# Kernel tuning notes

Measured on AMD Instinct MI355X. Metric: run time of the kernel, lower is better.

Reference implementation:

```python
import jax, jax.numpy as jnp
import numpy as np

EMBED_DIM = 1024
NUM_HEADS = 16
HEAD_DIM = EMBED_DIM // NUM_HEADS


def setup_inputs() -> dict:
    key = jax.random.key(0)
    ks = jax.random.split(key, 9)
    s = 1.0 / np.sqrt(EMBED_DIM)
    x = jax.random.normal(ks[0], (2, 2048, EMBED_DIM), dtype=jnp.float32)
    Wq = jax.random.uniform(ks[1], (EMBED_DIM, EMBED_DIM), jnp.float32, -s, s)
    bq = jax.random.uniform(ks[2], (EMBED_DIM,), jnp.float32, -s, s)
    Wk = jax.random.uniform(ks[3], (EMBED_DIM, EMBED_DIM), jnp.float32, -s, s)
    bk = jax.random.uniform(ks[4], (EMBED_DIM,), jnp.float32, -s, s)
    Wv = jax.random.uniform(ks[5], (EMBED_DIM, EMBED_DIM), jnp.float32, -s, s)
    bv = jax.random.uniform(ks[6], (EMBED_DIM,), jnp.float32, -s, s)
    Wo = jax.random.uniform(ks[7], (EMBED_DIM, EMBED_DIM), jnp.float32, -s, s)
    bo = jax.random.uniform(ks[8], (EMBED_DIM,), jnp.float32, -s, s)
    return {"x": x, "Wq": Wq, "bq": bq, "Wk": Wk, "bk": bk,
            "Wv": Wv, "bv": bv, "Wo": Wo, "bo": bo}


def reference(x, Wq, bq, Wk, bk, Wv, bv, Wo, bo):
    B, S, E = x.shape
    H, D = NUM_HEADS, HEAD_DIM
    # Linear projections (torch Linear: y = x @ W.T + b; here W stored as [in,out])
    Q = (x @ Wq + bq).reshape(B, S, H, D).transpose(0, 2, 1, 3)  # [B,H,S,D]
    K = (x @ Wk + bk).reshape(B, S, H, D).transpose(0, 2, 1, 3)
    V = (x @ Wv + bv).reshape(B, S, H, D).transpose(0, 2, 1, 3)
    scale = jnp.sqrt(jnp.asarray(D, dtype=jnp.float32))
    energy = jnp.einsum("bhqd,bhkd->bhqk", Q, K) / scale  # [B,H,S,S]
    attn = jax.nn.softmax(energy, axis=-1)
    out = jnp.einsum("bhqk,bhkd->bhqd", attn, V)  # [B,H,S,D]
    out = out.transpose(0, 2, 1, 3).reshape(B, S, E)
    return out @ Wo + bo
```

## Files before the change

kernel.cpp:

```cpp
#include <hip/hip_runtime.h>
#include <cstdint>
#include <cstddef>

#define S_LEN 2048
#define NHEAD 16
#define HDIM  64
#define EMB   1024
#define MROWS 4096
#define KDIM  1024

typedef __bf16 bf16;
typedef unsigned int u32;
typedef __attribute__((ext_vector_type(8)))  __bf16 bf16x8;
typedef __attribute__((ext_vector_type(4)))  __bf16 bf16x4;
typedef __attribute__((ext_vector_type(4)))  float  f32x4;
typedef __attribute__((ext_vector_type(16))) float  f32x16;
typedef __attribute__((ext_vector_type(4)))  u32    u32x4;

__device__ __forceinline__ f32x4 mfma_16x16x32(bf16x8 a, bf16x8 b, f32x4 c) {
  return __builtin_amdgcn_mfma_f32_16x16x32_bf16(a, b, c, 0, 0, 0);
}
__device__ __forceinline__ f32x16 mfma32(bf16x8 a, bf16x8 b, f32x16 c) {
  return __builtin_amdgcn_mfma_f32_32x32x16_bf16(a, b, c, 0, 0, 0);
}
__device__ __forceinline__ u32 cvt_pk_bf16(float lo, float hi) {
  u32 r;
  asm("v_cvt_pk_bf16_f32 %0, %1, %2" : "=v"(r) : "v"(lo), "v"(hi));
  return r;
}
__device__ __forceinline__ f32x16 fz16() {
  f32x16 z;
#pragma unroll
  for (int i = 0; i < 16; i++) z[i] = 0.f;
  return z;
}

__device__ __forceinline__ void gload16(const bf16* g, void* lds_uniform) {
  __builtin_amdgcn_global_load_lds(
      (const __attribute__((address_space(1))) void*)g,
      (__attribute__((address_space(3))) void*)lds_uniform, 16, 0, 0);
}

__global__ void prep_x_kernel(const float* __restrict__ x, bf16* __restrict__ xb) {
  int idx = blockIdx.x * blockDim.x + threadIdx.x;
  const float4* x4 = (const float4*)x;
  float4 a = x4[idx * 2 + 0];
  float4 b = x4[idx * 2 + 1];
  bf16x8 v;
  v[0] = (bf16)a.x; v[1] = (bf16)a.y; v[2] = (bf16)a.z; v[3] = (bf16)a.w;
  v[4] = (bf16)b.x; v[5] = (bf16)b.y; v[6] = (bf16)b.z; v[7] = (bf16)b.w;
  *(bf16x8*)(xb + (size_t)idx * 8) = v;
}

__global__ void prep_w_kernel(const float* __restrict__ Wq, const float* __restrict__ Wk,
                              const float* __restrict__ Wv, const float* __restrict__ Wo,
                              bf16* __restrict__ wqkvt, bf16* __restrict__ wot) {
  __shared__ float tile[64][65];
  int mat = blockIdx.z;
  const float* W = (mat == 0) ? Wq : (mat == 1) ? Wk : (mat == 2) ? Wv : Wo;
  bf16* dst = (mat < 3) ? (wqkvt + (size_t)mat * 1024 * 1024) : wot;
  int k0 = blockIdx.x * 64, r0 = blockIdx.y * 64;
  int tid = threadIdx.x;
#pragma unroll
  for (int i = 0; i < 16; i++) {
    int idx = i * 256 + tid;
    int kk = idx >> 6, rr = idx & 63;
    tile[kk][rr] = W[(size_t)(k0 + kk) * 1024 + r0 + rr];
  }
  __syncthreads();
#pragma unroll
  for (int i = 0; i < 16; i++) {
    int idx = i * 256 + tid;
    int rr = idx >> 6, kk = idx & 63;
    dst[(size_t)(r0 + rr) * 1024 + k0 + kk] = (bf16)tile[kk][rr];
  }
}

template <int MODE>
__global__ __launch_bounds__(256, 2) void gemm_bt(
    const bf16* __restrict__ A, const bf16* __restrict__ Bt,
    const float* __restrict__ b0, const float* __restrict__ b1, const float* __restrict__ b2,
    float* __restrict__ outf,
    bf16* __restrict__ qo, bf16* __restrict__ ko, bf16* __restrict__ vto) {
  __shared__ bf16 lA[128 * 64];
  __shared__ bf16 lB[128 * 64];
  const int bm = blockIdx.x, bn = blockIdx.y;
  const int tid = threadIdx.x;
  const int w = tid >> 6, l = tid & 63;
  const int wm = w >> 1, wn = w & 1;
  const int lr = l & 15, lg = l >> 4;

  f32x4 zero = {0.f, 0.f, 0.f, 0.f};
  f32x4 acc[4][4];
#pragma unroll
  for (int i = 0; i < 4; i++)
#pragma unroll
    for (int j = 0; j < 4; j++) acc[i][j] = zero;

  char* lAb = (char*)lA;
  char* lBb = (char*)lB;
  const size_t a_row0 = (size_t)bm * 128;
  const size_t b_row0 = (size_t)bn * 128;

  for (int kt = 0; kt < KDIM; kt += 64) {
    __syncthreads();
#pragma unroll
    for (int i = 0; i < 4; i++) {
      int cq = i * 256 + tid;
      int row = cq >> 3;
      int c8 = (cq & 7) ^ (row & 7);
      gload16(A + (a_row0 + row) * KDIM + kt + c8 * 8, lAb + (i * 256 + w * 64) * 16);
    }
#pragma unroll
    for (int i = 0; i < 4; i++) {
      int cq = i * 256 + tid;
      int row = cq >> 3;
      int c8 = (cq & 7) ^ (row & 7);
      gload16(Bt + (b_row0 + row) * KDIM + kt + c8 * 8, lBb + (i * 256 + w * 64) * 16);
    }
    asm volatile("s_waitcnt vmcnt(0)" ::: "memory");
    __syncthreads();

#pragma unroll
    for (int kk = 0; kk < 2; kk++) {
      bf16x8 af[4], bfv[4];
#pragma unroll
      for (int i = 0; i < 4; i++) {
        int row = wm * 64 + i * 16 + lr;
        af[i] = *(const bf16x8*)(lAb + row * 128 + ((((kk << 2) + lg) ^ (row & 7)) << 4));
      }
#pragma unroll
      for (int j = 0; j < 4; j++) {
        int row = wn * 64 + j * 16 + lr;
        bfv[j] = *(const bf16x8*)(lBb + row * 128 + ((((kk << 2) + lg) ^ (row & 7)) << 4));
      }
#pragma unroll
      for (int i = 0; i < 4; i++)
#pragma unroll
        for (int j = 0; j < 4; j++) acc[i][j] = mfma_16x16x32(af[i], bfv[j], acc[i][j]);
    }
  }

#pragma unroll
  for (int i = 0; i < 4; i++) {
#pragma unroll
    for (int j = 0; j < 4; j++) {
      int n = bn * 128 + wn * 64 + j * 16 + lr;
      int mbase = bm * 128 + wm * 64 + i * 16 + lg * 4;
      if (MODE == 1) {
#pragma unroll
        for (int jj = 0; jj < 4; jj++)
          outf[(size_t)(mbase + jj) * 1024 + n] = acc[i][j][jj] + b0[n];
      } else {
        int p = n >> 10, nn = n & 1023;
        int h = nn >> 6, d = nn & 63;
        int b = mbase >> 11, s = mbase & 2047;
        const float* bp = (p == 0) ? b0 : (p == 1) ? b1 : b2;
        float bias = bp[nn];
        if (p == 2) {
          bf16x4 pk;
#pragma unroll
          for (int jj = 0; jj < 4; jj++) pk[jj] = (bf16)(acc[i][j][jj] + bias);
          *(bf16x4*)(vto + (((size_t)(b * 16 + h)) * 64 + d) * 2048 + s) = pk;
        } else {
          float qsc = (p == 0) ? 0.18033688011112042f : 1.0f;
          bf16* o = (p == 0) ? qo : ko;
#pragma unroll
          for (int jj = 0; jj < 4; jj++)
            o[(((size_t)(b * 16 + h)) * 2048 + s + jj) * 64 + d] =
                (bf16)((acc[i][j][jj] + bias) * qsc);
        }
      }
    }
  }
}

__global__ __launch_bounds__(128, 2) void attn_kernel(
    const bf16* __restrict__ qb, const bf16* __restrict__ kb,
    const bf16* __restrict__ vtb, bf16* __restrict__ ob) {
  __shared__ bf16 lK[2 * 64 * 64];
  __shared__ bf16 lV[2 * 64 * 64];
  const int qt = blockIdx.x;
  const int bh = blockIdx.y;
  const int tid = threadIdx.x;
  const int w = tid >> 6, l = tid & 63;
  const int l5 = l >> 5, l31 = l & 31;

  const bf16* Qh = qb + (size_t)bh * S_LEN * HDIM;
  const bf16* Kh = kb + (size_t)bh * S_LEN * HDIM;
  const bf16* Vh = vtb + (size_t)bh * HDIM * S_LEN;

  const int qrow = qt * 64 + w * 32 + l31;
  const bf16* qp = Qh + (size_t)qrow * 64 + l5 * 8;
  bf16x8 qf0 = *(const bf16x8*)(qp);
  bf16x8 qf1 = *(const bf16x8*)(qp + 16);
  bf16x8 qf2 = *(const bf16x8*)(qp + 32);
  bf16x8 qf3 = *(const bf16x8*)(qp + 48);

  bf16x8 ones;
#pragma unroll
  for (int i = 0; i < 8; i++) ones[i] = (bf16)1.0f;

  f32x16 o0 = fz16(), o1 = fz16(), lsum = fz16();

  char* lKb = (char*)lK;
  char* lVb = (char*)lV;

  const int rb = l31 * 128;
  const int cso0 = (((0 + l5) ^ (l & 7)) << 4);
  const int cso1 = (((2 + l5) ^ (l & 7)) << 4);
  const int cso2 = (((4 + l5) ^ (l & 7)) << 4);
  const int cso3 = (((6 + l5) ^ (l & 7)) << 4);

  const int row0 = tid >> 3;
  const int c8b = ((tid & 7) ^ (row0 & 7)) << 3;
  int koff = row0 * HDIM + c8b;
  int voff = row0 * S_LEN + c8b;
  char* lkd = lKb + w * 1024;
  char* lvd = lVb + w * 1024;

#define STAGE(B)                                                              \
  {                                                                           \
    gload16(Kh + koff,         lkd + (B));                                    \
    gload16(Kh + koff + 1024,  lkd + (B) + 2048);                             \
    gload16(Kh + koff + 2048,  lkd + (B) + 4096);                             \
    gload16(Kh + koff + 3072,  lkd + (B) + 6144);                             \
    gload16(Vh + voff,         lvd + (B));                                    \
    gload16(Vh + voff + 32768, lvd + (B) + 2048);                             \
    gload16(Vh + voff + 65536, lvd + (B) + 4096);                             \
    gload16(Vh + voff + 98304, lvd + (B) + 6144);                             \
    koff += 4096;                                                             \
    voff += 64;                                                               \
  }

#define QKHALF(B, H, paA, paB)                                                \
  {                                                                           \
    const char* kB_ = lKb + (B) + (H) * 4096;                                 \
    f32x16 s = fz16();                                                        \
    __builtin_amdgcn_s_setprio(1);                                            \
    bf16x8 kf0 = *(const bf16x8*)(kB_ + rb + cso0);                           \
    bf16x8 kf1 = *(const bf16x8*)(kB_ + rb + cso1);                           \
    bf16x8 kf2 = *(const bf16x8*)(kB_ + rb + cso2);                           \
    bf16x8 kf3 = *(const bf16x8*)(kB_ + rb + cso3);                           \
    s = mfma32(kf0, qf0, s);                                                  \
    s = mfma32(kf1, qf1, s);                                                  \
    s = mfma32(kf2, qf2, s);                                                  \
    s = mfma32(kf3, qf3, s);                                                  \
    __builtin_amdgcn_s_setprio(0);                                            \
    _Pragma("unroll") for (int r = 0; r < 16; r++)                            \
      s[r] = __builtin_amdgcn_exp2f(s[r]);                                    \
    {                                                                         \
      u32 a_ = cvt_pk_bf16(s[0], s[1]);                                       \
      u32 b_ = cvt_pk_bf16(s[2], s[3]);                                       \
      u32 c_ = cvt_pk_bf16(s[4], s[5]);                                       \
      u32 d_ = cvt_pk_bf16(s[6], s[7]);                                       \
      asm("v_permlane32_swap_b32 %0, %1" : "+v"(a_), "+v"(c_));               \
      asm("v_permlane32_swap_b32 %0, %1" : "+v"(b_), "+v"(d_));               \
      u32x4 t_ = {a_, b_, c_, d_};                                            \
      paA = __builtin_bit_cast(bf16x8, t_);                                   \
    }                                                                         \
    {                                                                         \
      u32 a_ = cvt_pk_bf16(s[8], s[9]);                                       \
      u32 b_ = cvt_pk_bf16(s[10], s[11]);                                     \
      u32 c_ = cvt_pk_bf16(s[12], s[13]);                                     \
      u32 d_ = cvt_pk_bf16(s[14], s[15]);                                     \
      asm("v_permlane32_swap_b32 %0, %1" : "+v"(a_), "+v"(c_));               \
      asm("v_permlane32_swap_b32 %0, %1" : "+v"(b_), "+v"(d_));               \
      u32x4 t_ = {a_, b_, c_, d_};                                            \
      paB = __builtin_bit_cast(bf16x8, t_);                                   \
    }                                                                         \
  }

#define COMPUTE(B)                                                            \
  {                                                                           \
    bf16x8 pa0, pa1, pa2, pa3;                                                \
    QKHALF(B, 0, pa0, pa1);                                                   \
    QKHALF(B, 1, pa2, pa3);                                                   \
    const char* vB_ = lVb + (B);                                              \
    __builtin_amdgcn_s_setprio(1);                                            \
    lsum = mfma32(pa0, ones, lsum);                                           \
    lsum = mfma32(pa1, ones, lsum);                                           \
    lsum = mfma32(pa2, ones, lsum);                                           \
    lsum = mfma32(pa3, ones, lsum);                                           \
    {                                                                         \
      bf16x8 vf0 = *(const bf16x8*)(vB_ + rb + cso0);                         \
      bf16x8 vf1 = *(const bf16x8*)(vB_ + rb + cso1);                         \
      bf16x8 vf2 = *(const bf16x8*)(vB_ + rb + cso2);                         \
      bf16x8 vf3 = *(const bf16x8*)(vB_ + rb + cso3);                         \
      o0 = mfma32(pa0, vf0, o0);                                              \
      o0 = mfma32(pa1, vf1, o0);                                              \
      o0 = mfma32(pa2, vf2, o0);                                              \
      o0 = mfma32(pa3, vf3, o0);                                              \
    }                                                                         \
    {                                                                         \
      bf16x8 vf0 = *(const bf16x8*)(vB_ + 4096 + rb + cso0);                  \
      bf16x8 vf1 = *(const bf16x8*)(vB_ + 4096 + rb + cso1);                  \
      bf16x8 vf2 = *(const bf16x8*)(vB_ + 4096 + rb + cso2);                  \
      bf16x8 vf3 = *(const bf16x8*)(vB_ + 4096 + rb + cso3);                  \
      o1 = mfma32(pa0, vf0, o1);                                              \
      o1 = mfma32(pa1, vf1, o1);                                              \
      o1 = mfma32(pa2, vf2, o1);                                              \
      o1 = mfma32(pa3, vf3, o1);                                              \
    }                                                                         \
    __builtin_amdgcn_s_setprio(0);                                            \
  }

#define SYNC                                                                  \
  asm volatile("s_waitcnt vmcnt(0)" ::: "memory");                            \
  __syncthreads();

  STAGE(0);
  SYNC;

  for (int t = 0; t < 30; t += 2) {
    STAGE(8192);
    COMPUTE(0);
    SYNC;
    STAGE(0);
    COMPUTE(8192);
    SYNC;
  }
  STAGE(8192);
  COMPUTE(0);
  SYNC;
  COMPUTE(8192);

#undef STAGE
#undef QKHALF
#undef COMPUTE
#undef SYNC

  const int b = bh >> 4, h = bh & 15;
#pragma unroll
  for (int r = 0; r < 16; r++) {
    int q = (r & 3) + 8 * (r >> 2) + 4 * l5;
    int s = qt * 64 + w * 32 + q;
    float inv = 1.0f / lsum[r];
    size_t base = ((size_t)(b * 2048 + s)) * 1024 + h * 64 + l31;
    ob[base]      = (bf16)(o0[r] * inv);
    ob[base + 32] = (bf16)(o1[r] * inv);
  }
}

extern "C" void kernel_launch(void* const* d_in, const int* in_sizes, int n_in,
                              void* d_out, int out_size, void* d_ws, size_t ws_size,
                              hipStream_t stream) {
  const float* x  = (const float*)d_in[0];
  const float* Wq = (const float*)d_in[1];
  const float* bq = (const float*)d_in[2];
  const float* Wk = (const float*)d_in[3];
  const float* bk = (const float*)d_in[4];
  const float* Wv = (const float*)d_in[5];
  const float* bv = (const float*)d_in[6];
  const float* Wo = (const float*)d_in[7];
  const float* bo = (const float*)d_in[8];
  float* out = (float*)d_out;

  char* ws = (char*)d_ws;
  bf16* xb    = (bf16*)(ws + (size_t)(0)  * (1 << 20));
  bf16* wqkvt = (bf16*)(ws + (size_t)(8)  * (1 << 20));
  bf16* wot   = (bf16*)(ws + (size_t)(14) * (1 << 20));
  bf16* qbuf  = (bf16*)(ws + (size_t)(16) * (1 << 20));
  bf16* kbuf  = (bf16*)(ws + (size_t)(24) * (1 << 20));
  bf16* vtbuf = (bf16*)(ws + (size_t)(32) * (1 << 20));
  bf16* obuf  = (bf16*)(ws + (size_t)(40) * (1 << 20));

  prep_x_kernel<<<dim3(2048), dim3(256), 0, stream>>>(x, xb);
  prep_w_kernel<<<dim3(16, 16, 4), dim3(256), 0, stream>>>(Wq, Wk, Wv, Wo, wqkvt, wot);
  gemm_bt<0><<<dim3(32, 24), dim3(256), 0, stream>>>(xb, wqkvt, bq, bk, bv,
                                                     nullptr, qbuf, kbuf, vtbuf);
  attn_kernel<<<dim3(32, 32), dim3(128), 0, stream>>>(qbuf, kbuf, vtbuf, obuf);
  gemm_bt<1><<<dim3(32, 8), dim3(256), 0, stream>>>(obuf, wot, bo, nullptr, nullptr,
                                                    out, nullptr, nullptr, nullptr);
}
```

Before: 106.7 us.

## Widen attention blocks to 128 queries with 4-stage K/V prefetch and remapped grid

The attention kernel now uses 256 threads per block covering 128 query rows, so each K/V tile loaded into LDS is shared by four waves instead of two. The double buffer becomes a four-slot ring with three tiles prefetched ahead and partial vmcnt waits, so global loads overlap compute more deeply. A 1D grid with a swizzled block-to-work mapping groups blocks of the same head together for L2 reuse. LDS use rises to 64KB per block, which may limit occupancy.

```diff
diff --git a/kernel.cpp b/kernel.cpp
--- a/kernel.cpp
+++ b/kernel.cpp
@@ -175,13 +175,14 @@
   }
 }
 
-__global__ __launch_bounds__(128, 2) void attn_kernel(
+__global__ __launch_bounds__(256, 2) void attn_kernel(
     const bf16* __restrict__ qb, const bf16* __restrict__ kb,
     const bf16* __restrict__ vtb, bf16* __restrict__ ob) {
-  __shared__ bf16 lK[2 * 64 * 64];
-  __shared__ bf16 lV[2 * 64 * 64];
-  const int qt = blockIdx.x;
-  const int bh = blockIdx.y;
+  __shared__ bf16 lKV[4 * 8192];
+  const int bid = blockIdx.x;
+  const int work = ((bid & 7) << 6) | (bid >> 3);
+  const int qt = work & 15;
+  const int bh = work >> 4;
   const int tid = threadIdx.x;
   const int w = tid >> 6, l = tid & 63;
   const int l5 = l >> 5, l31 = l & 31;
@@ -190,7 +191,7 @@
   const bf16* Kh = kb + (size_t)bh * S_LEN * HDIM;
   const bf16* Vh = vtb + (size_t)bh * HDIM * S_LEN;
 
-  const int qrow = qt * 64 + w * 32 + l31;
+  const int qrow = qt * 128 + w * 32 + l31;
   const bf16* qp = Qh + (size_t)qrow * 64 + l5 * 8;
   bf16x8 qf0 = *(const bf16x8*)(qp);
   bf16x8 qf1 = *(const bf16x8*)(qp + 16);
@@ -203,8 +204,7 @@
 
   f32x16 o0 = fz16(), o1 = fz16(), lsum = fz16();
 
-  char* lKb = (char*)lK;
-  char* lVb = (char*)lV;
+  char* lb = (char*)lKV;
 
   const int rb = l31 * 128;
   const int cso0 = (((0 + l5) ^ (l & 7)) << 4);
@@ -213,29 +213,25 @@
   const int cso3 = (((6 + l5) ^ (l & 7)) << 4);
 
   const int row0 = tid >> 3;
-  const int c8b = ((tid & 7) ^ (row0 & 7)) << 3;
-  int koff = row0 * HDIM + c8b;
-  int voff = row0 * S_LEN + c8b;
-  char* lkd = lKb + w * 1024;
-  char* lvd = lVb + w * 1024;
+  const int c8e = (((tid & 7) ^ (row0 & 7)) << 3);
+  int koff = row0 * HDIM + c8e;
+  int voff = row0 * S_LEN + c8e;
+  char* lkd = lb + w * 1024;
+  char* lvd = lb + 8192 + w * 1024;
 
 #define STAGE(B)                                                              \
   {                                                                           \
     gload16(Kh + koff,         lkd + (B));                                    \
-    gload16(Kh + koff + 1024,  lkd + (B) + 2048);                             \
     gload16(Kh + koff + 2048,  lkd + (B) + 4096);                             \
-    gload16(Kh + koff + 3072,  lkd + (B) + 6144);                             \
     gload16(Vh + voff,         lvd + (B));                                    \
-    gload16(Vh + voff + 32768, lvd + (B) + 2048);                             \
     gload16(Vh + voff + 65536, lvd + (B) + 4096);                             \
-    gload16(Vh + voff + 98304, lvd + (B) + 6144);                             \
     koff += 4096;                                                             \
     voff += 64;                                                               \
   }
 
 #define QKHALF(B, H, paA, paB)                                                \
   {                                                                           \
-    const char* kB_ = lKb + (B) + (H) * 4096;                                 \
+    const char* kB_ = lb + (B) + (H) * 4096;                                  \
     f32x16 s = fz16();                                                        \
     __builtin_amdgcn_s_setprio(1);                                            \
     bf16x8 kf0 = *(const bf16x8*)(kB_ + rb + cso0);                           \
@@ -276,7 +272,7 @@
     bf16x8 pa0, pa1, pa2, pa3;                                                \
     QKHALF(B, 0, pa0, pa1);                                                   \
     QKHALF(B, 1, pa2, pa3);                                                   \
-    const char* vB_ = lVb + (B);                                              \
+    const char* vB_ = lb + (B) + 8192;                                        \
     __builtin_amdgcn_s_setprio(1);                                            \
     lsum = mfma32(pa0, ones, lsum);                                           \
     lsum = mfma32(pa1, ones, lsum);                                           \
@@ -305,36 +301,32 @@
     __builtin_amdgcn_s_setprio(0);                                            \
   }
 
-#define SYNC                                                                  \
-  asm volatile("s_waitcnt vmcnt(0)" ::: "memory");                            \
+  STAGE(0 << 14);
+  STAGE(1 << 14);
+  STAGE(2 << 14);
+
+  for (int t = 0; t < 30; ++t) {
+    asm volatile("s_waitcnt vmcnt(8)" ::: "memory");
+    __syncthreads();
+    if (t < 29) STAGE(((t + 3) & 3) << 14);
+    COMPUTE((t & 3) << 14);
+  }
+  asm volatile("s_waitcnt vmcnt(4)" ::: "memory");
   __syncthreads();
-
-  STAGE(0);
-  SYNC;
-
-  for (int t = 0; t < 30; t += 2) {
-    STAGE(8192);
-    COMPUTE(0);
-    SYNC;
-    STAGE(0);
-    COMPUTE(8192);
-    SYNC;
-  }
-  STAGE(8192);
-  COMPUTE(0);
-  SYNC;
-  COMPUTE(8192);
+  COMPUTE(2 << 14);
+  asm volatile("s_waitcnt vmcnt(0)" ::: "memory");
+  __syncthreads();
+  COMPUTE(3 << 14);
 
 #undef STAGE
 #undef QKHALF
 #undef COMPUTE
-#undef SYNC
 
   const int b = bh >> 4, h = bh & 15;
 #pragma unroll
   for (int r = 0; r < 16; r++) {
     int q = (r & 3) + 8 * (r >> 2) + 4 * l5;
-    int s = qt * 64 + w * 32 + q;
+    int s = qt * 128 + w * 32 + q;
     float inv = 1.0f / lsum[r];
     size_t base = ((size_t)(b * 2048 + s)) * 1024 + h * 64 + l31;
     ob[base]      = (bf16)(o0[r] * inv);
@@ -369,7 +361,7 @@
   prep_w_kernel<<<dim3(16, 16, 4), dim3(256), 0, stream>>>(Wq, Wk, Wv, Wo, wqkvt, wot);
   gemm_bt<0><<<dim3(32, 24), dim3(256), 0, stream>>>(xb, wqkvt, bq, bk, bv,
                                                      nullptr, qbuf, kbuf, vtbuf);
-  attn_kernel<<<dim3(32, 32), dim3(128), 0, stream>>>(qbuf, kbuf, vtbuf, obuf);
+  attn_kernel<<<dim3(512), dim3(256), 0, stream>>>(qbuf, kbuf, vtbuf, obuf);
   gemm_bt<1><<<dim3(32, 8), dim3(256), 0, stream>>>(obuf, wot, bo, nullptr, nullptr,
                                                     out, nullptr, nullptr, nullptr);
 }
```

Result: faster. 103.2 us (-3.4%).
